# Optimization experiments

Hardware: AMD Instinct MI355X
Metric: run time of the kernel (lower is better)

The kernel has to match this reference:

```python
import jax, jax.numpy as jnp
import numpy as np

DT = 1.0 / 200.0  # imu_freq = 200
EPS = 1e-8

def _skew(v):  # [B,3] -> [B,3,3]
    x, y, z = v[:, 0], v[:, 1], v[:, 2]
    zero = jnp.zeros_like(x)
    return jnp.stack([zero, -z, y, z, zero, -x, -y, x, zero], axis=-1).reshape(-1, 3, 3)

def _axis_angle_to_R(w, dt):
    # Rodrigues: R = I + sin(th) K + (1-cos(th)) K^2, th = ||w||*dt
    n = jnp.linalg.norm(w, axis=-1, keepdims=True)          # [B,1]
    theta = n[:, 0] * dt                                     # [B]
    axis = w / (n + EPS)
    K = _skew(axis)
    I = jnp.eye(3, dtype=w.dtype)
    s = jnp.sin(theta)[:, None, None]
    c = jnp.cos(theta)[:, None, None]
    return I + s * K + (1.0 - c) * jnp.einsum('bij,bjk->bik', K, K)

def _R_to_axis_angle(R):
    tr = jnp.trace(R, axis1=-2, axis2=-1)
    angle = jnp.arccos(jnp.clip((tr - 1.0) / 2.0, -1.0 + 1e-7, 1.0 - 1e-7))
    axis = jnp.stack([R[:, 2, 1] - R[:, 1, 2],
                      R[:, 0, 2] - R[:, 2, 0],
                      R[:, 1, 0] - R[:, 0, 1]], axis=-1)
    axis = axis / (2.0 * jnp.sin(angle)[:, None] + EPS)
    return axis, angle

def _aa_to_quat(axis, angle):  # (w, x, y, z)
    h = angle / 2.0
    return jnp.concatenate([jnp.cos(h)[:, None], axis * jnp.sin(h)[:, None]], axis=-1)

def setup_inputs() -> dict:
    key = jax.random.key(0)
    input_seq = jax.random.normal(key, (512, 4096, 6), dtype=jnp.float32)
    return {"input_seq": input_seq}

def reference(input_seq):
    B, T, _ = input_seq.shape
    dtype = input_seq.dtype
    w = jnp.transpose(input_seq[:, :, :3], (1, 0, 2))  # [T,B,3] gyro
    a = jnp.transpose(input_seq[:, :, 3:], (1, 0, 2))  # [T,B,3] accel
    dt = jnp.asarray(DT, dtype)
    dt2_half = dt * dt / 2.0

    dR0 = jnp.broadcast_to(jnp.eye(3, dtype=dtype), (B, 3, 3))
    dv0 = jnp.zeros((B, 3), dtype)
    dp0 = jnp.zeros((B, 3), dtype)

    def step(carry, inp):
        dR, dv, dp = carry
        w_k, a_k = inp
        dR = jnp.einsum('bij,bjk->bik', dR, _axis_angle_to_R(w_k, dt))
        Ra = jnp.einsum('bij,bj->bi', dR, a_k)
        dv = dv + Ra * dt
        dp = dp + dv * dt + Ra * dt2_half  # uses already-updated dv, as in torch code
        axis, angle = _R_to_axis_angle(dR)
        q = _aa_to_quat(axis, angle)
        return (dR, dv, dp), (dp, dv, q)

    _, (ps, vs, qs) = jax.lax.scan(step, (dR0, dv0, dp0), (w, a))
    ps = jnp.transpose(ps, (1, 0, 2))  # [B,T,3]
    vs = jnp.transpose(vs, (1, 0, 2))  # [B,T,3]
    qs = jnp.transpose(qs, (1, 0, 2))  # [B,T,4]
    return jnp.concatenate([input_seq, ps, qs, vs], axis=2)  # [B,T,16]
```

## Files before the change

kernel.cpp:

```cpp
#include <hip/hip_runtime.h>
#include <math.h>

#define T_LEN 4096
#define CHUNK 8
#define NTHR  512
#define ESTRIDE 15

__device__ __forceinline__ void make_A(float wx, float wy, float wz, float* A) {
    const float dt = 1.0f / 200.0f;
    float n = sqrtf(wx*wx + wy*wy + wz*wz);
    float theta = n * dt;
    float inv = 1.0f / (n + 1e-8f);
    float x = wx * inv, y = wy * inv, z = wz * inv;
    float s = sinf(theta);
    float c = cosf(theta);
    float oc = 1.0f - c;
    A[0] = 1.0f + oc * (-(y*y + z*z));
    A[1] = -s*z + oc * (x*y);
    A[2] =  s*y + oc * (x*z);
    A[3] =  s*z + oc * (x*y);
    A[4] = 1.0f + oc * (-(x*x + z*z));
    A[5] = -s*x + oc * (y*z);
    A[6] = -s*y + oc * (x*z);
    A[7] =  s*x + oc * (y*z);
    A[8] = 1.0f + oc * (-(x*x + y*y));
}

__device__ __forceinline__ void matmul3(const float* R, const float* A, float* N) {
#pragma unroll
    for (int i = 0; i < 3; ++i) {
        N[i*3+0] = R[i*3+0]*A[0] + R[i*3+1]*A[3] + R[i*3+2]*A[6];
        N[i*3+1] = R[i*3+0]*A[1] + R[i*3+1]*A[4] + R[i*3+2]*A[7];
        N[i*3+2] = R[i*3+0]*A[2] + R[i*3+1]*A[5] + R[i*3+2]*A[8];
    }
}

__device__ __forceinline__ void step(float* R, float* v, float* p,
                                     float wx, float wy, float wz,
                                     float ax, float ay, float az) {
    const float dt   = 1.0f / 200.0f;
    const float dt2h = dt * dt * 0.5f;
    float A[9], N[9];
    make_A(wx, wy, wz, A);
    matmul3(R, A, N);
#pragma unroll
    for (int i = 0; i < 9; ++i) R[i] = N[i];
    float rax = R[0]*ax + R[1]*ay + R[2]*az;
    float ray = R[3]*ax + R[4]*ay + R[5]*az;
    float raz = R[6]*ax + R[7]*ay + R[8]*az;
    v[0] += rax*dt; v[1] += ray*dt; v[2] += raz*dt;
    p[0] += v[0]*dt + rax*dt2h;
    p[1] += v[1]*dt + ray*dt2h;
    p[2] += v[2]*dt + raz*dt2h;
}

__global__ __launch_bounds__(NTHR)
void preint_kernel(const float* __restrict__ in, float* __restrict__ out) {
    const int b = blockIdx.x;
    const int t = threadIdx.x;
    const float dt = 1.0f / 200.0f;

    const float* bin  = in  + (size_t)b * T_LEN * 6;
    float*       bout = out + (size_t)b * T_LEN * 16;

    float in_reg[CHUNK * 6];
    {
        const float4* src4 = (const float4*)(bin + (size_t)t * CHUNK * 6);
#pragma unroll
        for (int i = 0; i < (CHUNK * 6) / 4; ++i) {
            float4 u = src4[i];
            in_reg[i*4+0] = u.x; in_reg[i*4+1] = u.y;
            in_reg[i*4+2] = u.z; in_reg[i*4+3] = u.w;
        }
    }

    float R[9] = {1,0,0, 0,1,0, 0,0,1};
    float v[3] = {0,0,0};
    float p[3] = {0,0,0};
#pragma unroll
    for (int k = 0; k < CHUNK; ++k) {
        const float* u = in_reg + k * 6;
        step(R, v, p, u[0], u[1], u[2], u[3], u[4], u[5]);
    }

    __shared__ float lds[NTHR * ESTRIDE];
    float* e = lds + t * ESTRIDE;
#pragma unroll
    for (int i = 0; i < 9; ++i) e[i] = R[i];
    e[9]  = v[0]; e[10] = v[1]; e[11] = v[2];
    e[12] = p[0]; e[13] = p[1]; e[14] = p[2];
    __syncthreads();

    for (int d = 1; d < NTHR; d <<= 1) {
        float L[15];
        const bool act = (t >= d);
        if (act) {
            const float* src = lds + (t - d) * ESTRIDE;
#pragma unroll
            for (int i = 0; i < 15; ++i) L[i] = src[i];
        }
        __syncthreads();
        if (act) {
            const float tau2 = (float)(d * CHUNK) * dt;
            float NA[9];
            matmul3(L, R, NA);
            float nb0 = L[9]  + L[0]*v[0] + L[1]*v[1] + L[2]*v[2];
            float nb1 = L[10] + L[3]*v[0] + L[4]*v[1] + L[5]*v[2];
            float nb2 = L[11] + L[6]*v[0] + L[7]*v[1] + L[8]*v[2];
            float nc0 = L[12] + tau2*L[9]  + L[0]*p[0] + L[1]*p[1] + L[2]*p[2];
            float nc1 = L[13] + tau2*L[10] + L[3]*p[0] + L[4]*p[1] + L[5]*p[2];
            float nc2 = L[14] + tau2*L[11] + L[6]*p[0] + L[7]*p[1] + L[8]*p[2];
#pragma unroll
            for (int i = 0; i < 9; ++i) R[i] = NA[i];
            v[0] = nb0; v[1] = nb1; v[2] = nb2;
            p[0] = nc0; p[1] = nc1; p[2] = nc2;
#pragma unroll
            for (int i = 0; i < 9; ++i) e[i] = R[i];
            e[9]  = v[0]; e[10] = v[1]; e[11] = v[2];
            e[12] = p[0]; e[13] = p[1]; e[14] = p[2];
        }
        __syncthreads();
    }

    float S[9]  = {1,0,0, 0,1,0, 0,0,1};
    float sv[3] = {0,0,0};
    float sp[3] = {0,0,0};
    if (t > 0) {
        const float* src = lds + (t - 1) * ESTRIDE;
#pragma unroll
        for (int i = 0; i < 9; ++i) S[i] = src[i];
        sv[0] = src[9];  sv[1] = src[10]; sv[2] = src[11];
        sp[0] = src[12]; sp[1] = src[13]; sp[2] = src[14];
    }

#pragma unroll
    for (int kk = 0; kk < CHUNK; kk += 2) {
        float4 row[8];
#pragma unroll
        for (int j = 0; j < 2; ++j) {
            const int k = kk + j;
            const float* u = in_reg + k * 6;
            step(S, sv, sp, u[0], u[1], u[2], u[3], u[4], u[5]);

            float tr  = S[0] + S[4] + S[8];
            float ca  = fminf(fmaxf(0.5f * (tr - 1.0f), -1.0f + 1e-7f), 1.0f - 1e-7f);
            float qw  = sqrtf(0.5f * (1.0f + ca));
            float i4  = 0.25f / qw;
            float qx  = (S[7] - S[5]) * i4;
            float qy  = (S[2] - S[6]) * i4;
            float qz  = (S[3] - S[1]) * i4;

            row[j*4+0] = make_float4(u[0], u[1], u[2], u[3]);
            row[j*4+1] = make_float4(u[4], u[5], sp[0], sp[1]);
            row[j*4+2] = make_float4(sp[2], qw, qx, qy);
            row[j*4+3] = make_float4(qz, sv[0], sv[1], sv[2]);
        }
        float4* orow = (float4*)(bout + (size_t)(t * CHUNK + kk) * 16);
#pragma unroll
        for (int i = 0; i < 8; ++i) orow[i] = row[i];
    }
}

extern "C" void kernel_launch(void* const* d_in, const int* in_sizes, int n_in,
                              void* d_out, int out_size, void* d_ws, size_t ws_size,
                              hipStream_t stream) {
    const float* in = (const float*)d_in[0];
    float* out = (float*)d_out;
    const int B = in_sizes[0] / (T_LEN * 6);
    preint_kernel<<<dim3(B), dim3(NTHR), 0, stream>>>(in, out);
}
```

Measured before the change: 207.3 us.

## Replace LDS Hillis-Steele scan with wave shuffle scan plus serial wave combine

Replaces the block-wide shared-memory scan, which has 9 barrier-separated rounds over 15-float elements, with an intra-wave shuffle scan followed by a single LDS exchange of the 8 per-wave totals. Each wave then serially composes the preceding wave totals. sin/cos of the small rotation angle are replaced by truncated Taylor polynomials. Inputs are no longer held in registers; they are reloaded from global memory as float2 in the second pass, which lowers register pressure at the cost of a second, likely cache-hit, read.

```diff
diff --git a/kernel.cpp b/kernel.cpp
--- a/kernel.cpp
+++ b/kernel.cpp
@@ -4,17 +4,18 @@
 #define T_LEN 4096
 #define CHUNK 8
 #define NTHR  512
-#define ESTRIDE 15
+#define NWAVE (NTHR / 64)
+#define DT    (1.0f / 200.0f)
 
 __device__ __forceinline__ void make_A(float wx, float wy, float wz, float* A) {
-    const float dt = 1.0f / 200.0f;
-    float n = sqrtf(wx*wx + wy*wy + wz*wz);
-    float theta = n * dt;
-    float inv = 1.0f / (n + 1e-8f);
-    float x = wx * inv, y = wy * inv, z = wz * inv;
-    float s = sinf(theta);
-    float c = cosf(theta);
-    float oc = 1.0f - c;
+    float nsq   = wx*wx + wy*wy + wz*wz;
+    float n     = sqrtf(nsq);
+    float theta = n * DT;
+    float inv   = 1.0f / (n + 1e-8f);
+    float x = wx*inv, y = wy*inv, z = wz*inv;
+    float t2 = theta * theta;
+    float s  = theta * (1.0f - t2 * (1.0f/6.0f)  * (1.0f - t2 * (1.0f/20.0f)));
+    float oc = t2 * 0.5f * (1.0f - t2 * (1.0f/12.0f) * (1.0f - t2 * (1.0f/30.0f)));
     A[0] = 1.0f + oc * (-(y*y + z*z));
     A[1] = -s*z + oc * (x*y);
     A[2] =  s*y + oc * (x*z);
@@ -38,8 +39,7 @@
 __device__ __forceinline__ void step(float* R, float* v, float* p,
                                      float wx, float wy, float wz,
                                      float ax, float ay, float az) {
-    const float dt   = 1.0f / 200.0f;
-    const float dt2h = dt * dt * 0.5f;
+    const float dt2h = DT * DT * 0.5f;
     float A[9], N[9];
     make_A(wx, wy, wz, A);
     matmul3(R, A, N);
@@ -48,90 +48,114 @@
     float rax = R[0]*ax + R[1]*ay + R[2]*az;
     float ray = R[3]*ax + R[4]*ay + R[5]*az;
     float raz = R[6]*ax + R[7]*ay + R[8]*az;
-    v[0] += rax*dt; v[1] += ray*dt; v[2] += raz*dt;
-    p[0] += v[0]*dt + rax*dt2h;
-    p[1] += v[1]*dt + ray*dt2h;
-    p[2] += v[2]*dt + raz*dt2h;
+    v[0] += rax*DT; v[1] += ray*DT; v[2] += raz*DT;
+    p[0] += v[0]*DT + rax*dt2h;
+    p[1] += v[1]*DT + ray*dt2h;
+    p[2] += v[2]*DT + raz*dt2h;
+}
+
+__device__ __forceinline__ void compose15(const float* L, const float* Rv,
+                                          float* O, float tau2) {
+    float NA[9];
+    matmul3(L, Rv, NA);
+    float nb0 = L[9]  + L[0]*Rv[9] + L[1]*Rv[10] + L[2]*Rv[11];
+    float nb1 = L[10] + L[3]*Rv[9] + L[4]*Rv[10] + L[5]*Rv[11];
+    float nb2 = L[11] + L[6]*Rv[9] + L[7]*Rv[10] + L[8]*Rv[11];
+    float nc0 = L[12] + tau2*L[9]  + L[0]*Rv[12] + L[1]*Rv[13] + L[2]*Rv[14];
+    float nc1 = L[13] + tau2*L[10] + L[3]*Rv[12] + L[4]*Rv[13] + L[5]*Rv[14];
+    float nc2 = L[14] + tau2*L[11] + L[6]*Rv[12] + L[7]*Rv[13] + L[8]*Rv[14];
+#pragma unroll
+    for (int i = 0; i < 9; ++i) O[i] = NA[i];
+    O[9] = nb0; O[10] = nb1; O[11] = nb2;
+    O[12] = nc0; O[13] = nc1; O[14] = nc2;
 }
 
 __global__ __launch_bounds__(NTHR)
 void preint_kernel(const float* __restrict__ in, float* __restrict__ out) {
-    const int b = blockIdx.x;
-    const int t = threadIdx.x;
-    const float dt = 1.0f / 200.0f;
+    const int b    = blockIdx.x;
+    const int t    = threadIdx.x;
+    const int lane = t & 63;
+    const int wid  = t >> 6;
 
     const float* bin  = in  + (size_t)b * T_LEN * 6;
     float*       bout = out + (size_t)b * T_LEN * 16;
+    const float2* cin2 = (const float2*)(bin + (size_t)t * CHUNK * 6);
 
-    float in_reg[CHUNK * 6];
+    float val[15];
     {
-        const float4* src4 = (const float4*)(bin + (size_t)t * CHUNK * 6);
+        float R[9] = {1,0,0, 0,1,0, 0,0,1};
+        float v[3] = {0,0,0};
+        float p[3] = {0,0,0};
 #pragma unroll
-        for (int i = 0; i < (CHUNK * 6) / 4; ++i) {
-            float4 u = src4[i];
-            in_reg[i*4+0] = u.x; in_reg[i*4+1] = u.y;
-            in_reg[i*4+2] = u.z; in_reg[i*4+3] = u.w;
+        for (int k = 0; k < CHUNK; ++k) {
+            float2 u0 = cin2[k*3+0];
+            float2 u1 = cin2[k*3+1];
+            float2 u2 = cin2[k*3+2];
+            step(R, v, p, u0.x, u0.y, u1.x, u1.y, u2.x, u2.y);
+        }
+#pragma unroll
+        for (int i = 0; i < 9; ++i) val[i] = R[i];
+        val[9]  = v[0]; val[10] = v[1]; val[11] = v[2];
+        val[12] = p[0]; val[13] = p[1]; val[14] = p[2];
+    }
+
+#pragma unroll
+    for (int d = 1; d < 64; d <<= 1) {
+        float L[15];
+#pragma unroll
+        for (int i = 0; i < 15; ++i) L[i] = __shfl_up(val[i], d, 64);
+        if (lane >= d) {
+            float O[15];
+            compose15(L, val, O, (float)(d * CHUNK) * DT);
+#pragma unroll
+            for (int i = 0; i < 15; ++i) val[i] = O[i];
         }
     }
 
-    float R[9] = {1,0,0, 0,1,0, 0,0,1};
-    float v[3] = {0,0,0};
-    float p[3] = {0,0,0};
+    __shared__ float wtot[NWAVE][16];
+    if (lane == 63) {
 #pragma unroll
-    for (int k = 0; k < CHUNK; ++k) {
-        const float* u = in_reg + k * 6;
-        step(R, v, p, u[0], u[1], u[2], u[3], u[4], u[5]);
+        for (int i = 0; i < 15; ++i) wtot[wid][i] = val[i];
+    }
+    __syncthreads();
+
+    float E[15];
+    if (wid > 0) {
+#pragma unroll
+        for (int i = 0; i < 15; ++i) E[i] = wtot[0][i];
+        const float tauW = (float)(64 * CHUNK) * DT;
+        for (int w = 1; w < wid; ++w) {
+            float Tw[15], O[15];
+#pragma unroll
+            for (int i = 0; i < 15; ++i) Tw[i] = wtot[w][i];
+            compose15(E, Tw, O, tauW);
+#pragma unroll
+            for (int i = 0; i < 15; ++i) E[i] = O[i];
+        }
     }
 
-    __shared__ float lds[NTHR * ESTRIDE];
-    float* e = lds + t * ESTRIDE;
+    float P[15];
 #pragma unroll
-    for (int i = 0; i < 9; ++i) e[i] = R[i];
-    e[9]  = v[0]; e[10] = v[1]; e[11] = v[2];
-    e[12] = p[0]; e[13] = p[1]; e[14] = p[2];
-    __syncthreads();
-
-    for (int d = 1; d < NTHR; d <<= 1) {
-        float L[15];
-        const bool act = (t >= d);
-        if (act) {
-            const float* src = lds + (t - d) * ESTRIDE;
+    for (int i = 0; i < 15; ++i) P[i] = __shfl_up(val[i], 1, 64);
+    if (lane == 0) {
+        P[0]=1; P[1]=0; P[2]=0; P[3]=0; P[4]=1; P[5]=0; P[6]=0; P[7]=0; P[8]=1;
 #pragma unroll
-            for (int i = 0; i < 15; ++i) L[i] = src[i];
-        }
-        __syncthreads();
-        if (act) {
-            const float tau2 = (float)(d * CHUNK) * dt;
-            float NA[9];
-            matmul3(L, R, NA);
-            float nb0 = L[9]  + L[0]*v[0] + L[1]*v[1] + L[2]*v[2];
-            float nb1 = L[10] + L[3]*v[0] + L[4]*v[1] + L[5]*v[2];
-            float nb2 = L[11] + L[6]*v[0] + L[7]*v[1] + L[8]*v[2];
-            float nc0 = L[12] + tau2*L[9]  + L[0]*p[0] + L[1]*p[1] + L[2]*p[2];
-            float nc1 = L[13] + tau2*L[10] + L[3]*p[0] + L[4]*p[1] + L[5]*p[2];
-            float nc2 = L[14] + tau2*L[11] + L[6]*p[0] + L[7]*p[1] + L[8]*p[2];
-#pragma unroll
-            for (int i = 0; i < 9; ++i) R[i] = NA[i];
-            v[0] = nb0; v[1] = nb1; v[2] = nb2;
-            p[0] = nc0; p[1] = nc1; p[2] = nc2;
-#pragma unroll
-            for (int i = 0; i < 9; ++i) e[i] = R[i];
-            e[9]  = v[0]; e[10] = v[1]; e[11] = v[2];
-            e[12] = p[0]; e[13] = p[1]; e[14] = p[2];
-        }
-        __syncthreads();
+        for (int i = 9; i < 15; ++i) P[i] = 0.0f;
     }
 
-    float S[9]  = {1,0,0, 0,1,0, 0,0,1};
-    float sv[3] = {0,0,0};
-    float sp[3] = {0,0,0};
-    if (t > 0) {
-        const float* src = lds + (t - 1) * ESTRIDE;
+    float X[15];
+    if (wid > 0) {
+        compose15(E, P, X, (float)(lane * CHUNK) * DT);
+    } else {
 #pragma unroll
-        for (int i = 0; i < 9; ++i) S[i] = src[i];
-        sv[0] = src[9];  sv[1] = src[10]; sv[2] = src[11];
-        sp[0] = src[12]; sp[1] = src[13]; sp[2] = src[14];
+        for (int i = 0; i < 15; ++i) X[i] = P[i];
     }
+
+    float S[9], sv[3], sp[3];
+#pragma unroll
+    for (int i = 0; i < 9; ++i) S[i] = X[i];
+    sv[0] = X[9];  sv[1] = X[10]; sv[2] = X[11];
+    sp[0] = X[12]; sp[1] = X[13]; sp[2] = X[14];
 
 #pragma unroll
     for (int kk = 0; kk < CHUNK; kk += 2) {
@@ -139,8 +163,10 @@
 #pragma unroll
         for (int j = 0; j < 2; ++j) {
             const int k = kk + j;
-            const float* u = in_reg + k * 6;
-            step(S, sv, sp, u[0], u[1], u[2], u[3], u[4], u[5]);
+            float2 u0 = cin2[k*3+0];
+            float2 u1 = cin2[k*3+1];
+            float2 u2 = cin2[k*3+2];
+            step(S, sv, sp, u0.x, u0.y, u1.x, u1.y, u2.x, u2.y);
 
             float tr  = S[0] + S[4] + S[8];
             float ca  = fminf(fmaxf(0.5f * (tr - 1.0f), -1.0f + 1e-7f), 1.0f - 1e-7f);
@@ -150,8 +176,8 @@
             float qy  = (S[2] - S[6]) * i4;
             float qz  = (S[3] - S[1]) * i4;
 
-            row[j*4+0] = make_float4(u[0], u[1], u[2], u[3]);
-            row[j*4+1] = make_float4(u[4], u[5], sp[0], sp[1]);
+            row[j*4+0] = make_float4(u0.x, u0.y, u1.x, u1.y);
+            row[j*4+1] = make_float4(u2.x, u2.y, sp[0], sp[1]);
             row[j*4+2] = make_float4(sp[2], qw, qx, qy);
             row[j*4+3] = make_float4(qz, sv[0], sv[1], sv[2]);
         }
```

Result: slower. 222.1 us (+7.1%).
